# Optimization experiments

Measured on AMD Instinct MI355X. Metric: run time of the kernel, lower is better.

Reference implementation:

```python
import jax, jax.numpy as jnp
import numpy as np

N = 50000     # nodes
E = 800000    # edges (before self-loops)
DIN = 128     # input feature dim
DH = 16       # per-head hidden dim (layer 1)
H = 8         # heads (layer 1)
DOUT = 64     # output classes (layer 2, heads=1)


def setup_inputs() -> dict:
    key = jax.random.key(0)
    ks = jax.random.split(key, 10)
    def rn(k, shape, scale=0.1):
        return jax.random.normal(k, shape, dtype=jnp.float32) * scale
    x = jax.random.normal(ks[0], (N, DIN), dtype=jnp.float32)
    edge_index = jax.random.randint(ks[1], (2, E), 0, N, dtype=jnp.int64)
    return {
        "x": x,
        "edge_index": edge_index,
        "W1": rn(ks[2], (DIN, H * DH)),
        "a_src1": rn(ks[3], (H, DH)),
        "a_dst1": rn(ks[4], (H, DH)),
        "b1": jnp.zeros((H * DH,), jnp.float32),
        "W2": rn(ks[5], (H * DH, DOUT)),
        "a_src2": rn(ks[6], (1, DOUT)),
        "a_dst2": rn(ks[7], (1, DOUT)),
        "b2": jnp.zeros((DOUT,), jnp.float32),
    }


def gat_conv(x, src, dst, W, a_src, a_dst, b, heads, out_dim):
    """PyG-style GATConv: edge attention + segment softmax over dst + scatter-add."""
    n = x.shape[0]
    h = (x @ W).reshape(n, heads, out_dim)                 # [N, H, D]
    alpha_src = jnp.sum(h * a_src, axis=-1)                # [N, H]
    alpha_dst = jnp.sum(h * a_dst, axis=-1)                # [N, H]
    e = jax.nn.leaky_relu(alpha_src[src] + alpha_dst[dst], 0.2)  # [Etot, H]
    # numerically-stable segment softmax grouped by destination node
    m = jax.ops.segment_max(e, dst, num_segments=n)        # [N, H]
    ex = jnp.exp(e - m[dst])
    s = jax.ops.segment_sum(ex, dst, num_segments=n)       # [N, H]
    alpha = ex / (s[dst] + 1e-16)                          # [Etot, H]
    msg = h[src] * alpha[..., None]                        # [Etot, H, D]
    out = jax.ops.segment_sum(msg, dst, num_segments=n)    # [N, H, D]
    return out.reshape(n, heads * out_dim) + b


def reference(x, W1, a_src1, a_dst1, b1, W2, a_src2, a_dst2, b2, edge_index):
    # eval mode: F.dropout(p=0.6, training=False) is identity
    loop = jnp.arange(N, dtype=edge_index.dtype)
    src = jnp.concatenate([edge_index[0], loop])  # add_self_loops=True (PyG default)
    dst = jnp.concatenate([edge_index[1], loop])
    h = gat_conv(x, src, dst, W1, a_src1, a_dst1, b1, H, DH)
    h = jax.nn.elu(h)
    h = gat_conv(h, src, dst, W2, a_src2, a_dst2, b2, 1, DOUT)
    return (h, jax.nn.log_softmax(h, axis=1))
```

## Files before the change

### kernel.cpp

```cpp
#include <hip/hip_runtime.h>

#define NN 50000
#define EE 800000
#define ET (EE + NN)
#define NCH ((NN + 255) / 256)
#define DEGB ((ET + 255) / 256)
#define WPB ((128 * 128 + 128 * 64 + 255) / 256)
#define GEMB ((NN + 63) / 64)

typedef unsigned short ushort_t;
using bf16x8 = __attribute__((ext_vector_type(8))) short;
using f32x4  = __attribute__((ext_vector_type(4))) float;

__device__ __forceinline__ float bf2f(ushort_t u) {
    return __uint_as_float(((unsigned int)u) << 16);
}
__device__ __forceinline__ ushort_t f2bf(float f) {
    unsigned int u = __float_as_uint(f);
    u += 0x7fffu + ((u >> 16) & 1u);
    return (ushort_t)(u >> 16);
}
__device__ __forceinline__ float lrelu(float e) {
    return fmaxf(e, 0.f) + 0.2f * fminf(e, 0.f);
}
__device__ __forceinline__ float ldf(const void* p, int i, bool f32) {
    return f32 ? ((const float*)p)[i] : bf2f(((const ushort_t*)p)[i]);
}

__device__ __forceinline__ bool sniff_f32(const unsigned int* __restrict__ xw) {
    int lane = threadIdx.x & 63;
    float v = __uint_as_float(xw[lane]);
    float a = fabsf(v);
    bool ok = (a > 1e-6f && a < 1e6f) || v == 0.f;
    unsigned long long m = __ballot(ok);
    return __popcll(m) >= 48;
}
__device__ __forceinline__ bool sniff_i64(const int* __restrict__ eiw) {
    int lane = threadIdx.x & 63;
    unsigned long long m = __ballot(eiw[2 * lane + 1] != 0);
    return __popcll(m) <= 4;
}

__device__ __forceinline__ void edge_sd(const int* ei, int i, bool i64, int& s, int& d) {
    if (i < EE) {
        if (i64) { s = ei[2 * i]; d = ei[2 * (EE + i)]; }
        else     { s = ei[i];     d = ei[EE + i]; }
    } else {
        s = d = i - EE;
    }
}
__device__ __forceinline__ int edge_d(const int* ei, int i, bool i64) {
    if (i < EE) return i64 ? ei[2 * (EE + i)] : ei[EE + i];
    return i - EE;
}

__global__ __launch_bounds__(256) void prep_kernel(const int* __restrict__ ei, int* __restrict__ deg8,
                                                   int* __restrict__ rank,
                                                   const unsigned int* __restrict__ xw,
                                                   const void* W1v, const void* W2v,
                                                   ushort_t* __restrict__ Wt1, ushort_t* __restrict__ Wt2) {
    int b = blockIdx.x;
    if (b < DEGB) {
        bool i64 = sniff_i64(ei);
        int i = b * 256 + threadIdx.x;
        if (i >= ET) return;
        int g = b & 7;
        int d = edge_d(ei, i, i64);
        rank[i] = atomicAdd(&deg8[(size_t)g * NN + d], 1);
    } else {
        bool f32 = sniff_f32(xw);
        int i = (b - DEGB) * 256 + threadIdx.x;
        if (i < 128 * 128) {
            int k = i >> 7, nc = i & 127;
            ushort_t v = f32 ? f2bf(((const float*)W1v)[i]) : ((const ushort_t*)W1v)[i];
            Wt1[nc * 128 + k] = v;
        }
        int j = i - 128 * 128;
        if (j >= 0 && j < 128 * 64) {
            int k = j >> 6, nc = j & 63;
            ushort_t v = f32 ? f2bf(((const float*)W2v)[j]) : ((const ushort_t*)W2v)[j];
            Wt2[nc * 128 + k] = v;
        }
    }
}

#define FLG_A (1ull << 62)

__global__ __launch_bounds__(256) void scan_kernel(int* __restrict__ deg8, int* __restrict__ rowptr,
                                                   unsigned long long* __restrict__ state) {
    __shared__ int wsum[4];
    __shared__ int bpref;
    int b = blockIdx.x;
    int t = threadIdx.x;
    int node = b * 256 + t;
    int lane = t & 63, wid = t >> 6;
    int dv[8];
    int v = 0;
    if (node < NN) {
        #pragma unroll
        for (int g = 0; g < 8; ++g) {
            dv[g] = deg8[(size_t)g * NN + node];
            v += dv[g];
        }
    }
    int x = v;
    #pragma unroll
    for (int off = 1; off < 64; off <<= 1) {
        int y = __shfl_up(x, off);
        if (lane >= off) x += y;
    }
    if (lane == 63) wsum[wid] = x;
    __syncthreads();
    if (t < 4) {
        int s = wsum[t];
        #pragma unroll
        for (int off = 1; off < 4; off <<= 1) {
            int y = __shfl_up(s, off);
            if (t >= off) s += y;
        }
        wsum[t] = s;
    }
    __syncthreads();
    int total = wsum[3];
    if (t == 0) atomicExch(&state[b], FLG_A | (unsigned long long)(unsigned)total);
    if (t < 64) {
        int p = 0;
        #pragma unroll
        for (int w = 0; w < (NCH + 63) / 64; ++w) {
            int j = w * 64 + t;
            unsigned long long sv = 0;
            if (j < b) {
                do { sv = atomicAdd(&state[j], 0ull); __builtin_amdgcn_s_sleep(1); } while (!(sv >> 62));
            }
            p += (int)(unsigned)(sv & 0xffffffffull);
        }
        #pragma unroll
        for (int off = 1; off < 64; off <<= 1) p += __shfl_xor(p, off);
        if (t == 0) bpref = p;
    }
    __syncthreads();
    int excl = x - v + ((wid > 0) ? wsum[wid - 1] : 0);
    if (node < NN) {
        int run = bpref + excl;
        rowptr[node] = run;
        #pragma unroll
        for (int g = 0; g < 8; ++g) {
            deg8[(size_t)g * NN + node] = run;
            run += dv[g];
        }
    }
    if (b == NCH - 1 && t == 0) rowptr[NN] = bpref + total;
}

template <bool AEXT, int NCOL, int NH>
__device__ __forceinline__ void mgemm_body(int bid, const void* Av, const ushort_t* __restrict__ Wt,
                                           const void* a_src, const void* a_dst,
                                           ushort_t* __restrict__ outb, float* __restrict__ asrc,
                                           float* __restrict__ adst, int n, bool f32) {
    constexpr int K = 128;
    constexpr int NCT = NCOL / 16;
    bool af32 = AEXT && f32;
    int t = threadIdx.x;
    int lane = t & 63, wid = t >> 6;
    int m = lane & 15, quad = lane >> 4;
    int rbase = bid * 64 + wid * 16;
    int row = rbase + m;
    bool rok = row < n;

    bf16x8 af[4];
    if (rok) {
        if (!af32) {
            const ushort_t* ap = (const ushort_t*)Av + (size_t)row * K + quad * 8;
            #pragma unroll
            for (int kk = 0; kk < 4; ++kk) af[kk] = *(const bf16x8*)(ap + kk * 32);
        } else {
            const float* ap = (const float*)Av + (size_t)row * K + quad * 8;
            #pragma unroll
            for (int kk = 0; kk < 4; ++kk) {
                float4 q0 = *(const float4*)(ap + kk * 32);
                float4 q1 = *(const float4*)(ap + kk * 32 + 4);
                bf16x8 v;
                v[0] = (short)f2bf(q0.x); v[1] = (short)f2bf(q0.y);
                v[2] = (short)f2bf(q0.z); v[3] = (short)f2bf(q0.w);
                v[4] = (short)f2bf(q1.x); v[5] = (short)f2bf(q1.y);
                v[6] = (short)f2bf(q1.z); v[7] = (short)f2bf(q1.w);
                af[kk] = v;
            }
        }
    } else {
        #pragma unroll
        for (int kk = 0; kk < 4; ++kk) af[kk] = (bf16x8){0, 0, 0, 0, 0, 0, 0, 0};
    }

    f32x4 acc[NCT];
    #pragma unroll
    for (int c = 0; c < NCT; ++c) acc[c] = (f32x4){0.f, 0.f, 0.f, 0.f};

    const ushort_t* wp = Wt + (size_t)m * K + quad * 8;
    #pragma unroll
    for (int c = 0; c < NCT; ++c) {
        const ushort_t* wc = wp + (size_t)c * 16 * K;
        #pragma unroll
        for (int kk = 0; kk < 4; ++kk) {
            bf16x8 bf = *(const bf16x8*)(wc + kk * 32);
            acc[c] = __builtin_amdgcn_mfma_f32_16x16x32_bf16(af[kk], bf, acc[c], 0, 0, 0);
        }
    }

    int orow0 = rbase + quad * 4;
    #pragma unroll
    for (int c = 0; c < NCT; ++c) {
        #pragma unroll
        for (int r = 0; r < 4; ++r) {
            int orow = orow0 + r;
            if (orow < n) outb[(size_t)orow * NCOL + c * 16 + m] = f2bf(acc[c][r]);
        }
    }

    if (NH == 8) {
        #pragma unroll
        for (int c = 0; c < NCT; ++c) {
            float as = ldf(a_src, c * 16 + m, f32);
            float ad = ldf(a_dst, c * 16 + m, f32);
            float ps[4], pd[4];
            #pragma unroll
            for (int r = 0; r < 4; ++r) { ps[r] = acc[c][r] * as; pd[r] = acc[c][r] * ad; }
            #pragma unroll
            for (int stp = 1; stp < 16; stp <<= 1) {
                #pragma unroll
                for (int r = 0; r < 4; ++r) {
                    ps[r] += __shfl_xor(ps[r], stp);
                    pd[r] += __shfl_xor(pd[r], stp);
                }
            }
            if (m == 0) {
                #pragma unroll
                for (int r = 0; r < 4; ++r) {
                    int orow = orow0 + r;
                    if (orow < n) {
                        asrc[(size_t)orow * 8 + c] = ps[r];
                        adst[(size_t)orow * 8 + c] = pd[r];
                    }
                }
            }
        }
    } else {
        float ps[4] = {0.f, 0.f, 0.f, 0.f}, pd[4] = {0.f, 0.f, 0.f, 0.f};
        #pragma unroll
        for (int c = 0; c < NCT; ++c) {
            float as = ldf(a_src, c * 16 + m, f32);
            float ad = ldf(a_dst, c * 16 + m, f32);
            #pragma unroll
            for (int r = 0; r < 4; ++r) {
                ps[r] = fmaf(acc[c][r], as, ps[r]);
                pd[r] = fmaf(acc[c][r], ad, pd[r]);
            }
        }
        #pragma unroll
        for (int stp = 1; stp < 16; stp <<= 1) {
            #pragma unroll
            for (int r = 0; r < 4; ++r) {
                ps[r] += __shfl_xor(ps[r], stp);
                pd[r] += __shfl_xor(pd[r], stp);
            }
        }
        if (m == 0) {
            #pragma unroll
            for (int r = 0; r < 4; ++r) {
                int orow = orow0 + r;
                if (orow < n) { asrc[orow] = ps[r]; adst[orow] = pd[r]; }
            }
        }
    }
}

__global__ __launch_bounds__(256) void gemm1_fill_kernel(const void* xv, const ushort_t* __restrict__ Wt1,
                                                         const void* as1, const void* ad1,
                                                         ushort_t* __restrict__ h1b,
                                                         float* __restrict__ asrc1, float* __restrict__ adst1,
                                                         const int* __restrict__ ei,
                                                         const int* __restrict__ deg8off,
                                                         const int* __restrict__ rank, int* __restrict__ col) {
    if (blockIdx.x < GEMB) {
        bool f32 = sniff_f32((const unsigned int*)xv);
        mgemm_body<true, 128, 8>(blockIdx.x, xv, Wt1, as1, ad1, h1b, asrc1, adst1, NN, f32);
        return;
    }
    int bb = blockIdx.x - GEMB;
    bool i64 = sniff_i64(ei);
    int i = bb * 256 + threadIdx.x;
    if (i >= ET) return;
    int g = bb & 7;
    int s, d;
    edge_sd(ei, i, i64, s, d);
    col[deg8off[(size_t)g * NN + d] + rank[i]] = s;
}

__global__ __launch_bounds__(256) void mgemm2_kernel(const void* Av, const ushort_t* __restrict__ Wt,
                                                     const void* a_src, const void* a_dst,
                                                     ushort_t* __restrict__ outb, float* __restrict__ asrc,
                                                     float* __restrict__ adst, const unsigned int* __restrict__ xw) {
    bool f32 = sniff_f32(xw);
    mgemm_body<false, 64, 1>(blockIdx.x, Av, Wt, a_src, a_dst, outb, asrc, adst, NN, f32);
}

__global__ __launch_bounds__(256) void agg1_kernel(const unsigned int* __restrict__ xw,
                                                   const int* __restrict__ rowptr, const int* __restrict__ col,
                                                   const ushort_t* __restrict__ h1b,
                                                   const float* __restrict__ asrc, const float* __restrict__ adst,
                                                   const void* b1, ushort_t* __restrict__ hmidb) {
    __shared__ float wle[4][8 * 72];
    __shared__ int loff[4][64];
    bool f32 = sniff_f32(xw);
    int lane = threadIdx.x & 63, wid = threadIdx.x >> 6;
    int d = blockIdx.x * 4 + wid;
    if (d >= NN) return;
    int start = rowptr[d], end = rowptr[d + 1];
    int hB = lane >> 3;
    const float4* dp = (const float4*)(adst + (size_t)d * 8);
    float4 ad0 = dp[0], ad1 = dp[1];
    const char* hb = (const char*)h1b + lane * 4;
    float acc0 = 0.f, acc1 = 0.f, ssum = 0.f;
    for (int chunk = start; chunk < end; chunk += 64) {
        int cnt = min(64, end - chunk);
        int c = (chunk + lane < end) ? col[chunk + lane] : 0;
        loff[wid][lane] = c << 8;
        if (lane < cnt) {
            const float4* ap = (const float4*)(asrc + (size_t)c * 8);
            float4 s0 = ap[0], s1 = ap[1];
            wle[wid][0 * 72 + lane] = __expf(lrelu(s0.x + ad0.x));
            wle[wid][1 * 72 + lane] = __expf(lrelu(s0.y + ad0.y));
            wle[wid][2 * 72 + lane] = __expf(lrelu(s0.z + ad0.z));
            wle[wid][3 * 72 + lane] = __expf(lrelu(s0.w + ad0.w));
            wle[wid][4 * 72 + lane] = __expf(lrelu(s1.x + ad1.x));
            wle[wid][5 * 72 + lane] = __expf(lrelu(s1.y + ad1.y));
            wle[wid][6 * 72 + lane] = __expf(lrelu(s1.z + ad1.z));
            wle[wid][7 * 72 + lane] = __expf(lrelu(s1.w + ad1.w));
        }
        #pragma unroll 8
        for (int j = 0; j < cnt; ++j) {
            int off = loff[wid][j];
            float ex = wle[wid][hB * 72 + j];
            unsigned int hv = *(const unsigned int*)(hb + off);
            ssum += ex;
            acc0 = fmaf(ex, __uint_as_float(hv << 16), acc0);
            acc1 = fmaf(ex, __uint_as_float(hv & 0xffff0000u), acc1);
        }
    }
    float inv = 1.f / (ssum + 1e-16f);
    float o0 = fmaf(acc0, inv, ldf(b1, lane * 2, f32));
    float o1 = fmaf(acc1, inv, ldf(b1, lane * 2 + 1, f32));
    o0 = (o0 > 0.f) ? o0 : (__expf(o0) - 1.f);
    o1 = (o1 > 0.f) ? o1 : (__expf(o1) - 1.f);
    unsigned int pk = ((unsigned int)f2bf(o1) << 16) | (unsigned int)f2bf(o0);
    *(unsigned int*)(hmidb + (size_t)d * 128 + lane * 2) = pk;
}

__global__ __launch_bounds__(256) void agg2_kernel(const unsigned int* __restrict__ xw,
                                                   const int* __restrict__ rowptr, const int* __restrict__ col,
                                                   const ushort_t* __restrict__ h2b,
                                                   const float* __restrict__ asrc, const float* __restrict__ adst,
                                                   const void* b2, float* __restrict__ out) {
    __shared__ float wle[4][64];
    __shared__ int loff[4][64];
    bool f32 = sniff_f32(xw);
    int lane = threadIdx.x & 63, wid = threadIdx.x >> 6;
    int d = blockIdx.x * 4 + wid;
    if (d >= NN) return;
    int start = rowptr[d], end = rowptr[d + 1];
    float ad = adst[d];
    const char* hb = (const char*)h2b + lane * 2;
    float acc = 0.f, ssum = 0.f;
    for (int chunk = start; chunk < end; chunk += 64) {
        int cnt = min(64, end - chunk);
        int c = (chunk + lane < end) ? col[chunk + lane] : 0;
        loff[wid][lane] = c << 7;
        if (lane < cnt) wle[wid][lane] = __expf(lrelu(asrc[c] + ad));
        #pragma unroll 8
        for (int j = 0; j < cnt; ++j) {
            int off = loff[wid][j];
            float ex = wle[wid][j];
            float hv = bf2f(*(const ushort_t*)(hb + off));
            ssum += ex;
            acc = fmaf(ex, hv, acc);
        }
    }
    float o = acc / (ssum + 1e-16f) + ldf(b2, lane, f32);
    float mm = o;
    #pragma unroll
    for (int off = 1; off < 64; off <<= 1) mm = fmaxf(mm, __shfl_xor(mm, off));
    float texp = __expf(o - mm);
    float ts = texp;
    #pragma unroll
    for (int off = 1; off < 64; off <<= 1) ts += __shfl_xor(ts, off);
    float ls = o - mm - __logf(ts);
    out[(size_t)d * 64 + lane] = o;
    out[(size_t)NN * 64 + (size_t)d * 64 + lane] = ls;
}

extern "C" void kernel_launch(void* const* d_in, const int* in_sizes, int n_in,
                              void* d_out, int out_size, void* d_ws, size_t ws_size,
                              hipStream_t stream) {
    const void* x   = d_in[0];
    const int*  ei  = (const int*)d_in[1];
    const void* W1  = d_in[2];
    const void* as1 = d_in[3];
    const void* ad1 = d_in[4];
    const void* b1  = d_in[5];
    const void* W2  = d_in[6];
    const void* as2 = d_in[7];
    const void* ad2 = d_in[8];
    const void* b2  = d_in[9];
    float* out = (float*)d_out;

    char* w = (char*)d_ws;
    auto alloc = [&](size_t bytes) {
        void* p = (void*)w;
        w += (bytes + 255) & ~(size_t)255;
        return p;
    };
    int* deg8     = (int*)alloc((size_t)8 * NN * 4 + 4096);
    unsigned long long* state = (unsigned long long*)((char*)deg8 + (size_t)8 * NN * 4);
    int* rowptr   = (int*)alloc((size_t)(NN + 1) * 4);
    int* rank     = (int*)alloc((size_t)ET * 4);
    int* colx     = (int*)alloc((size_t)ET * 4);
    ushort_t* Wt1 = (ushort_t*)alloc((size_t)128 * 128 * 2);
    ushort_t* Wt2 = (ushort_t*)alloc((size_t)64 * 128 * 2);
    ushort_t* h1b = (ushort_t*)alloc((size_t)NN * 128 * 2);
    float* asrc1  = (float*)alloc((size_t)NN * 8 * 4);
    float* adst1  = (float*)alloc((size_t)NN * 8 * 4);
    ushort_t* hmidb = (ushort_t*)alloc((size_t)NN * 128 * 2);
    ushort_t* h2b = (ushort_t*)alloc((size_t)NN * 64 * 2);
    float* asrc2  = (float*)alloc((size_t)NN * 4);
    float* adst2  = (float*)alloc((size_t)NN * 4);

    hipMemsetAsync(deg8, 0, (size_t)8 * NN * 4 + (size_t)NCH * 8, stream);

    prep_kernel<<<DEGB + WPB, 256, 0, stream>>>(ei, deg8, rank, (const unsigned int*)x, W1, W2, Wt1, Wt2);
    scan_kernel<<<NCH, 256, 0, stream>>>(deg8, rowptr, state);
    gemm1_fill_kernel<<<GEMB + DEGB, 256, 0, stream>>>(x, Wt1, as1, ad1, h1b, asrc1, adst1,
                                                       ei, deg8, rank, colx);
    agg1_kernel<<<(NN + 3) / 4, 256, 0, stream>>>((const unsigned int*)x, rowptr, colx, h1b,
                                                  asrc1, adst1, b1, hmidb);
    mgemm2_kernel<<<GEMB, 256, 0, stream>>>((const void*)hmidb, Wt2, as2, ad2, h2b, asrc2, adst2,
                                            (const unsigned int*)x);
    agg2_kernel<<<(NN + 3) / 4, 256, 0, stream>>>((const unsigned int*)x, rowptr, colx, h2b,
                                                  asrc2, adst2, b2, out);
}
```

Baseline: 253.4 us.

## Process multiple edges per wavefront with 16-byte gathers in both aggregation kernels

Both aggregation kernels now split each wavefront into lane groups that each handle a different edge, with every lane loading 16 bytes (8 bf16 features) per neighbor instead of 2 or 4 bytes. Partial sums are combined with xor-shuffles across groups, and one group applies the epilogue. In agg2 the log-softmax is computed per lane over 8 values, then reduced across lanes, and results are written as float4. The aim is fewer serial iterations over neighbors and wider memory transactions. The cost is more registers, padding zeros for unused edge slots, and reductions across lane groups.

```diff
diff --git a/kernel.cpp b/kernel.cpp
--- a/kernel.cpp
+++ b/kernel.cpp
@@ -316,11 +316,14 @@
     int d = blockIdx.x * 4 + wid;
     if (d >= NN) return;
     int start = rowptr[d], end = rowptr[d + 1];
-    int hB = lane >> 3;
+    int sub = lane & 15;
+    int eg  = lane >> 4;
+    int hB  = sub >> 1;
     const float4* dp = (const float4*)(adst + (size_t)d * 8);
     float4 ad0 = dp[0], ad1 = dp[1];
-    const char* hb = (const char*)h1b + lane * 4;
-    float acc0 = 0.f, acc1 = 0.f, ssum = 0.f;
+    const char* hb = (const char*)h1b + sub * 16;
+    float acc[8] = {0.f, 0.f, 0.f, 0.f, 0.f, 0.f, 0.f, 0.f};
+    float ssum = 0.f;
     for (int chunk = start; chunk < end; chunk += 64) {
         int cnt = min(64, end - chunk);
         int c = (chunk + lane < end) ? col[chunk + lane] : 0;
@@ -336,24 +339,49 @@
             wle[wid][5 * 72 + lane] = __expf(lrelu(s1.y + ad1.y));
             wle[wid][6 * 72 + lane] = __expf(lrelu(s1.z + ad1.z));
             wle[wid][7 * 72 + lane] = __expf(lrelu(s1.w + ad1.w));
-        }
-        #pragma unroll 8
-        for (int j = 0; j < cnt; ++j) {
+        } else {
+            #pragma unroll
+            for (int h = 0; h < 8; ++h) wle[wid][h * 72 + lane] = 0.f;
+        }
+        int niter = (cnt + 3) >> 2;
+        #pragma unroll 4
+        for (int jj = 0; jj < niter; ++jj) {
+            int j = jj * 4 + eg;
             int off = loff[wid][j];
             float ex = wle[wid][hB * 72 + j];
-            unsigned int hv = *(const unsigned int*)(hb + off);
+            uint4 hv = *(const uint4*)(hb + off);
             ssum += ex;
-            acc0 = fmaf(ex, __uint_as_float(hv << 16), acc0);
-            acc1 = fmaf(ex, __uint_as_float(hv & 0xffff0000u), acc1);
-        }
-    }
-    float inv = 1.f / (ssum + 1e-16f);
-    float o0 = fmaf(acc0, inv, ldf(b1, lane * 2, f32));
-    float o1 = fmaf(acc1, inv, ldf(b1, lane * 2 + 1, f32));
-    o0 = (o0 > 0.f) ? o0 : (__expf(o0) - 1.f);
-    o1 = (o1 > 0.f) ? o1 : (__expf(o1) - 1.f);
-    unsigned int pk = ((unsigned int)f2bf(o1) << 16) | (unsigned int)f2bf(o0);
-    *(unsigned int*)(hmidb + (size_t)d * 128 + lane * 2) = pk;
+            acc[0] = fmaf(ex, __uint_as_float(hv.x << 16), acc[0]);
+            acc[1] = fmaf(ex, __uint_as_float(hv.x & 0xffff0000u), acc[1]);
+            acc[2] = fmaf(ex, __uint_as_float(hv.y << 16), acc[2]);
+            acc[3] = fmaf(ex, __uint_as_float(hv.y & 0xffff0000u), acc[3]);
+            acc[4] = fmaf(ex, __uint_as_float(hv.z << 16), acc[4]);
+            acc[5] = fmaf(ex, __uint_as_float(hv.z & 0xffff0000u), acc[5]);
+            acc[6] = fmaf(ex, __uint_as_float(hv.w << 16), acc[6]);
+            acc[7] = fmaf(ex, __uint_as_float(hv.w & 0xffff0000u), acc[7]);
+        }
+    }
+    #pragma unroll
+    for (int off = 16; off < 64; off <<= 1) {
+        ssum += __shfl_xor(ssum, off);
+        #pragma unroll
+        for (int k = 0; k < 8; ++k) acc[k] += __shfl_xor(acc[k], off);
+    }
+    if (eg == 0) {
+        float inv = 1.f / (ssum + 1e-16f);
+        uint4 pk;
+        unsigned int pw[4];
+        #pragma unroll
+        for (int k = 0; k < 4; ++k) {
+            float o0 = fmaf(acc[2 * k],     inv, ldf(b1, sub * 8 + 2 * k,     f32));
+            float o1 = fmaf(acc[2 * k + 1], inv, ldf(b1, sub * 8 + 2 * k + 1, f32));
+            o0 = (o0 > 0.f) ? o0 : (__expf(o0) - 1.f);
+            o1 = (o1 > 0.f) ? o1 : (__expf(o1) - 1.f);
+            pw[k] = ((unsigned int)f2bf(o1) << 16) | (unsigned int)f2bf(o0);
+        }
+        pk.x = pw[0]; pk.y = pw[1]; pk.z = pw[2]; pk.w = pw[3];
+        *(uint4*)(hmidb + (size_t)d * 128 + sub * 8) = pk;
+    }
 }
 
 __global__ __launch_bounds__(256) void agg2_kernel(const unsigned int* __restrict__ xw,
@@ -368,34 +396,71 @@
     int d = blockIdx.x * 4 + wid;
     if (d >= NN) return;
     int start = rowptr[d], end = rowptr[d + 1];
+    int sub = lane & 7;
+    int eg  = lane >> 3;
     float ad = adst[d];
-    const char* hb = (const char*)h2b + lane * 2;
-    float acc = 0.f, ssum = 0.f;
+    const char* hb = (const char*)h2b + sub * 16;
+    float acc[8] = {0.f, 0.f, 0.f, 0.f, 0.f, 0.f, 0.f, 0.f};
+    float ssum = 0.f;
     for (int chunk = start; chunk < end; chunk += 64) {
         int cnt = min(64, end - chunk);
         int c = (chunk + lane < end) ? col[chunk + lane] : 0;
         loff[wid][lane] = c << 7;
-        if (lane < cnt) wle[wid][lane] = __expf(lrelu(asrc[c] + ad));
-        #pragma unroll 8
-        for (int j = 0; j < cnt; ++j) {
+        float e = 0.f;
+        if (lane < cnt) e = __expf(lrelu(asrc[c] + ad));
+        wle[wid][lane] = e;
+        int niter = (cnt + 7) >> 3;
+        #pragma unroll 2
+        for (int jj = 0; jj < niter; ++jj) {
+            int j = jj * 8 + eg;
             int off = loff[wid][j];
             float ex = wle[wid][j];
-            float hv = bf2f(*(const ushort_t*)(hb + off));
+            uint4 hv = *(const uint4*)(hb + off);
             ssum += ex;
-            acc = fmaf(ex, hv, acc);
-        }
-    }
-    float o = acc / (ssum + 1e-16f) + ldf(b2, lane, f32);
-    float mm = o;
+            acc[0] = fmaf(ex, __uint_as_float(hv.x << 16), acc[0]);
+            acc[1] = fmaf(ex, __uint_as_float(hv.x & 0xffff0000u), acc[1]);
+            acc[2] = fmaf(ex, __uint_as_float(hv.y << 16), acc[2]);
+            acc[3] = fmaf(ex, __uint_as_float(hv.y & 0xffff0000u), acc[3]);
+            acc[4] = fmaf(ex, __uint_as_float(hv.z << 16), acc[4]);
+            acc[5] = fmaf(ex, __uint_as_float(hv.z & 0xffff0000u), acc[5]);
+            acc[6] = fmaf(ex, __uint_as_float(hv.w << 16), acc[6]);
+            acc[7] = fmaf(ex, __uint_as_float(hv.w & 0xffff0000u), acc[7]);
+        }
+    }
     #pragma unroll
-    for (int off = 1; off < 64; off <<= 1) mm = fmaxf(mm, __shfl_xor(mm, off));
-    float texp = __expf(o - mm);
-    float ts = texp;
-    #pragma unroll
-    for (int off = 1; off < 64; off <<= 1) ts += __shfl_xor(ts, off);
-    float ls = o - mm - __logf(ts);
-    out[(size_t)d * 64 + lane] = o;
-    out[(size_t)NN * 64 + (size_t)d * 64 + lane] = ls;
+    for (int off = 8; off < 64; off <<= 1) {
+        ssum += __shfl_xor(ssum, off);
+        #pragma unroll
+        for (int k = 0; k < 8; ++k) acc[k] += __shfl_xor(acc[k], off);
+    }
+    if (eg == 0) {
+        float inv = 1.f / (ssum + 1e-16f);
+        float o[8];
+        #pragma unroll
+        for (int k = 0; k < 8; ++k) o[k] = fmaf(acc[k], inv, ldf(b2, sub * 8 + k, f32));
+        float mm = o[0];
+        #pragma unroll
+        for (int k = 1; k < 8; ++k) mm = fmaxf(mm, o[k]);
+        #pragma unroll
+        for (int off = 1; off < 8; off <<= 1) mm = fmaxf(mm, __shfl_xor(mm, off));
+        float ts = 0.f;
+        #pragma unroll
+        for (int k = 0; k < 8; ++k) ts += __expf(o[k] - mm);
+        #pragma unroll
+        for (int off = 1; off < 8; off <<= 1) ts += __shfl_xor(ts, off);
+        float lg = mm + __logf(ts);
+        float4 w0, w1, l0, l1;
+        w0.x = o[0]; w0.y = o[1]; w0.z = o[2]; w0.w = o[3];
+        w1.x = o[4]; w1.y = o[5]; w1.z = o[6]; w1.w = o[7];
+        l0.x = o[0] - lg; l0.y = o[1] - lg; l0.z = o[2] - lg; l0.w = o[3] - lg;
+        l1.x = o[4] - lg; l1.y = o[5] - lg; l1.z = o[6] - lg; l1.w = o[7] - lg;
+        float* op = out + (size_t)d * 64 + sub * 8;
+        *(float4*)op = w0;
+        *(float4*)(op + 4) = w1;
+        float* lp = out + (size_t)NN * 64 + (size_t)d * 64 + sub * 8;
+        *(float4*)lp = l0;
+        *(float4*)(lp + 4) = l1;
+    }
 }
 
 extern "C" void kernel_launch(void* const* d_in, const int* in_sizes, int n_in,
```

Result: no change. 252.0 us (-0.6%).
